# Performance work log

Hardware: AMD Instinct MI355X
Metric: run time of the kernel (lower is better)

## Reference

```python
import jax, jax.numpy as jnp
import numpy as np

IN_CH, PATCH, STRIDE, RES, NCLS = 3, 64, 32, 4096, 1000
SPECTRAL_RADIUS = 0.9


def setup_inputs() -> dict:
    key = jax.random.key(0)
    ks = jax.random.split(key, 8)
    x = jax.random.normal(ks[0], (128, IN_CH, 8224), dtype=jnp.float32)
    # Conv1d weights: [out=PATCH, in=IN_CH, k=PATCH]
    fan_in = IN_CH * PATCH
    bound = 1.0 / np.sqrt(fan_in)
    conv_w = jax.random.uniform(ks[1], (PATCH, IN_CH, PATCH), minval=-bound, maxval=bound, dtype=jnp.float32)
    conv_b = jax.random.uniform(ks[2], (PATCH,), minval=-bound, maxval=bound, dtype=jnp.float32)
    # Reservoir weights (uniform(-0.5, 0.5)), spectral-radius normalized
    rng = np.random.default_rng(0)
    Wres = rng.random((RES, RES), dtype=np.float32) - 0.5
    max_eig = np.max(np.abs(np.linalg.eigvals(Wres)))
    Wres = Wres * (SPECTRAL_RADIUS / max_eig)
    W_reservoir = jnp.asarray(Wres, dtype=jnp.float32)
    W_input = jax.random.uniform(ks[3], (RES, PATCH), minval=-0.5, maxval=0.5, dtype=jnp.float32)
    # cls/dist tokens init to zeros (as in torch)
    cls_token = jnp.zeros((1, PATCH), dtype=jnp.float32)
    dist_token = jnp.zeros((1, PATCH), dtype=jnp.float32)
    hb = 1.0 / np.sqrt(RES)
    w_cls = jax.random.uniform(ks[4], (NCLS, RES), minval=-hb, maxval=hb, dtype=jnp.float32)
    b_cls = jax.random.uniform(ks[5], (NCLS,), minval=-hb, maxval=hb, dtype=jnp.float32)
    w_dist = jax.random.uniform(ks[6], (NCLS, RES), minval=-hb, maxval=hb, dtype=jnp.float32)
    b_dist = jax.random.uniform(ks[7], (NCLS,), minval=-hb, maxval=hb, dtype=jnp.float32)
    return {"x": x, "conv_w": conv_w, "conv_b": conv_b, "W_reservoir": W_reservoir,
            "W_input": W_input, "cls_token": cls_token, "dist_token": dist_token,
            "w_cls": w_cls, "b_cls": b_cls, "w_dist": w_dist, "b_dist": b_dist}


def reference(x, conv_w, conv_b, W_reservoir, W_input, cls_token, dist_token,
              w_cls, b_cls, w_dist, b_dist):
    B = x.shape[0]
    # PatchEmbed: conv1d -> [B, PATCH, L]
    feat = jax.lax.conv_general_dilated(
        x, conv_w, window_strides=(STRIDE,), padding='VALID',
        dimension_numbers=('NCH', 'OIH', 'NCH')) + conv_b[None, :, None]
    WinT = W_input.T  # [PATCH, RES]
    us = jnp.transpose(feat, (2, 0, 1))  # [L, B, PATCH]
    h0 = jnp.zeros((B, RES), dtype=x.dtype)

    def step(h, u):
        h = jnp.tanh(h @ W_reservoir + u @ WinT)
        return h, None

    h, _ = jax.lax.scan(step, h0, us)
    cls_tok = jnp.broadcast_to(cls_token, (B, PATCH))
    dist_tok = jnp.broadcast_to(dist_token, (B, PATCH))
    h_cls = jnp.tanh(h @ W_reservoir + cls_tok @ WinT)
    h_dist = jnp.tanh(h @ W_reservoir + dist_tok @ WinT)
    cls_out = h_cls @ w_cls.T + b_cls
    dist_out = h_dist @ w_dist.T + b_dist
    # eval mode: log_softmax of the averaged logits
    return jax.nn.log_softmax((cls_out + dist_out) * 0.5, axis=1)
```

## Files before the change

kernel.cpp:

```cpp
#include <hip/hip_runtime.h>
#include <hip/hip_bf16.h>

#define LSTEPS 256

typedef short  bf16x8_t  __attribute__((ext_vector_type(8)));
typedef float  f32x4_t   __attribute__((ext_vector_type(4)));
typedef unsigned short us4_t __attribute__((ext_vector_type(4)));
typedef unsigned short us8_t __attribute__((ext_vector_type(8)));

static __device__ __forceinline__ unsigned short f2bf(float f) {
  unsigned int u = __float_as_uint(f);
  unsigned int r = (u + 0x7fffu + ((u >> 16) & 1u)) >> 16;
  return (unsigned short)r;
}
static __device__ __forceinline__ float bf2f(unsigned short s) {
  return __uint_as_float(((unsigned int)s) << 16);
}
static __device__ __forceinline__ float tanh_fast(float x) {
  float e = __expf(2.f * x);
  return 1.f - 2.f / (e + 1.f);
}

#define GLD(dst, off, sbase)                                              \
  asm volatile("global_load_dwordx4 %0, %1, %2 sc0"                       \
               : "=v"(dst)                                                \
               : "v"(off), "s"(sbase)                                     \
               : "memory");

__global__ __launch_bounds__(256) void prep_wc_kernel(
    const float* __restrict__ wcls, const float* __restrict__ wdist,
    unsigned short* __restrict__ Wcat)
{
  const int row = blockIdx.x;
  const float* src = nullptr;
  if (row < 1000) src = wcls + (size_t)row * 4096;
  else if (row >= 1024 && row < 2024) src = wdist + (size_t)(row - 1024) * 4096;
  unsigned short* dst = Wcat + (size_t)row * 4096;
  #pragma unroll 4
  for (int r = 0; r < 16; ++r) {
    const int c = r * 256 + threadIdx.x;
    dst[c] = src ? f2bf(src[c]) : (unsigned short)0;
  }
}

__global__ __launch_bounds__(256) void conv_kernel(
    const float* __restrict__ x, const float* __restrict__ w,
    const float* __restrict__ bias, unsigned short* __restrict__ U)
{
  __shared__ float wl[192][64];
  const int b  = blockIdx.x >> 4;
  const int tg = blockIdx.x & 15;
  const int tid = threadIdx.x;
  for (int i = tid; i < 64 * 192; i += 256)
    wl[i % 192][i / 192] = w[i];
  __syncthreads();
  const int wv = tid >> 6, p = tid & 63;
  const float* xb = x + (size_t)b * (3 * 8224);
  const float bp = bias[p];
  for (int tt = 0; tt < 4; ++tt) {
    const int t = tg * 16 + wv * 4 + tt;
    float acc = bp;
    const float* xw = xb + t * 32;
    #pragma unroll
    for (int c = 0; c < 3; ++c)
      #pragma unroll 8
      for (int k = 0; k < 64; ++k)
        acc += xw[c * 8224 + k] * wl[c * 64 + k][p];
    U[((size_t)t * 8 + (p >> 3)) * 1024 + (size_t)b * 8 + (p & 7)] = f2bf(acc);
  }
}

__global__ __launch_bounds__(256) void prep_tok_kernel(
    const float* __restrict__ cls, const float* __restrict__ dist,
    unsigned short* __restrict__ U)
{
  const int i = blockIdx.x * 256 + threadIdx.x;
  const int s = i >> 13, rem = i & 8191;
  const int kg = rem >> 10, e = rem & 7;
  const float* tok = s ? dist : cls;
  U[(size_t)(256 + s) * 8192 + rem] = f2bf(tok[kg * 8 + e]);
}

__global__ __launch_bounds__(512, 1) void reservoir_persistent(
    const float* __restrict__ wres,
    const unsigned short* __restrict__ U,
    const float* __restrict__ winp,
    unsigned short* __restrict__ A0, unsigned short* __restrict__ A1,
    unsigned short* __restrict__ Hcls, unsigned short* __restrict__ Hdist,
    unsigned int* __restrict__ lcnt, unsigned int* __restrict__ gcnt,
    unsigned int* __restrict__ lgo)
{
  extern __shared__ char smem[];
  unsigned short* Wl = (unsigned short*)smem;

  const int bid  = blockIdx.x;
  const int tid  = threadIdx.x;
  const int w    = tid >> 6;
  const int lane = tid & 63;
  const int q    = lane >> 4;
  const int l15  = lane & 15;
  const int grp  = bid & 7;
  const int nbase = bid * 16;

  {
    const int c4 = (tid & 3) * 4;
    for (int k = tid >> 2; k < 4096; k += 128) {
      float4 v = *(const float4*)(wres + (size_t)k * 4096 + nbase + c4);
      unsigned short* dst = Wl + ((k >> 3) * 16 + c4) * 8 + (k & 7);
      dst[0]  = f2bf(v.x); dst[8]  = f2bf(v.y);
      dst[16] = f2bf(v.z); dst[24] = f2bf(v.w);
    }
    if (tid < 128) {
      const int kg_u = tid >> 4, col = tid & 15;
      const float* src = winp + (size_t)(nbase + col) * 64 + kg_u * 8;
      unsigned short* dst = Wl + ((512 + kg_u) * 16 + col) * 8;
      #pragma unroll
      for (int e = 0; e < 8; ++e) dst[e] = f2bf(src[e]);
    }
  }
  __syncthreads();

  const unsigned int vbase = (unsigned int)(q * 2048 + (w * 16 + l15) * 16);
  unsigned int phase = 0;

#define ISSUE_A(BUF, CO)                                                     \
  { const unsigned int o_ = vbase + (unsigned int)(CO) * 32768u;             \
    GLD(BUF[0], o_, Ar);                                                     \
    GLD(BUF[1], o_ + 8192u, Ar);                                             \
    GLD(BUF[2], o_ + 16384u, Ar);                                            \
    GLD(BUF[3], o_ + 24576u, Ar); }

#define ISSUE_U(BUF)                                                         \
  { GLD(BUF[0], vbase, Ut);                                                  \
    GLD(BUF[1], vbase + 8192u, Ut); }

#define MMW(BUF, CI, VN)                                                     \
  { const unsigned short* wp_ = Wl + (unsigned int)(CI) * 2048 + q * 128 + l15 * 8; \
    bf16x8_t w0_ = *(const bf16x8_t*)(wp_);                                  \
    bf16x8_t w1_ = *(const bf16x8_t*)(wp_ + 512);                            \
    bf16x8_t w2_ = *(const bf16x8_t*)(wp_ + 1024);                           \
    bf16x8_t w3_ = *(const bf16x8_t*)(wp_ + 1536);                           \
    asm volatile("s_waitcnt vmcnt(" #VN ")" ::: "memory");                   \
    __builtin_amdgcn_sched_barrier(0);                                       \
    acc = __builtin_amdgcn_mfma_f32_16x16x32_bf16(BUF[0], w0_, acc, 0, 0, 0);\
    acc = __builtin_amdgcn_mfma_f32_16x16x32_bf16(BUF[1], w1_, acc, 0, 0, 0);\
    acc = __builtin_amdgcn_mfma_f32_16x16x32_bf16(BUF[2], w2_, acc, 0, 0, 0);\
    acc = __builtin_amdgcn_mfma_f32_16x16x32_bf16(BUF[3], w3_, acc, 0, 0, 0); }

  #pragma unroll 1
  for (int t = 0; t < LSTEPS + 2; ++t) {
    const unsigned short* Arp = (t <= LSTEPS) ? ((t & 1) ? A1 : A0) : A0;
    unsigned short* Awp = ((t + 1) & 1) ? A1 : A0;
    const unsigned long long Ar = (unsigned long long)Arp;
    const unsigned long long Ut = (unsigned long long)(U + (size_t)t * 8192);

    f32x4_t acc = (f32x4_t){0.f, 0.f, 0.f, 0.f};
    bf16x8_t b0[4], b1[4], b2[4];

    ISSUE_A(b0, 0); ISSUE_A(b1, 1); ISSUE_A(b2, 2);

    int ci = 0;
    #pragma unroll 1
    for (int ii = 0; ii < 9; ++ii) {
      MMW(b0, ci,     8); ISSUE_A(b0, ci + 3);
      MMW(b1, ci + 1, 8); ISSUE_A(b1, ci + 4);
      MMW(b2, ci + 2, 8); ISSUE_A(b2, ci + 5);
      ci += 3;
    }
    MMW(b0, 27, 8); ISSUE_A(b0, 30);
    MMW(b1, 28, 8); ISSUE_A(b1, 31);
    MMW(b2, 29, 8); ISSUE_U(b2);
    MMW(b0, 30, 6);
    MMW(b1, 31, 2);
    {
      const unsigned short* wp_ = Wl + 65536 + q * 128 + l15 * 8;
      bf16x8_t w0_ = *(const bf16x8_t*)(wp_);
      bf16x8_t w1_ = *(const bf16x8_t*)(wp_ + 512);
      asm volatile("s_waitcnt vmcnt(0)" ::: "memory");
      __builtin_amdgcn_sched_barrier(0);
      acc = __builtin_amdgcn_mfma_f32_16x16x32_bf16(b2[0], w0_, acc, 0, 0, 0);
      acc = __builtin_amdgcn_mfma_f32_16x16x32_bf16(b2[1], w1_, acc, 0, 0, 0);
    }

    {
      const int grow = w * 16 + q * 4;
      if (t < LSTEPS) {
        const int kg_out = bid * 2 + (l15 >> 3);
        unsigned short* dst = Awp + ((size_t)kg_out * 128 + grow) * 8 + (l15 & 7);
        dst[0]  = f2bf(tanh_fast(acc[0]));
        dst[8]  = f2bf(tanh_fast(acc[1]));
        dst[16] = f2bf(tanh_fast(acc[2]));
        dst[24] = f2bf(tanh_fast(acc[3]));
      } else {
        unsigned short* H = (t == LSTEPS) ? Hcls : Hdist;
        unsigned short* dst = H + (size_t)grow * 4096 + nbase + l15;
        dst[0]     = f2bf(tanh_fast(acc[0]));
        dst[4096]  = f2bf(tanh_fast(acc[1]));
        dst[8192]  = f2bf(tanh_fast(acc[2]));
        dst[12288] = f2bf(tanh_fast(acc[3]));
      }
    }

    phase += 1;
    __syncthreads();
    if (tid == 0) {
      unsigned int prev = __hip_atomic_fetch_add(&lcnt[grp * 32], 1u,
                            __ATOMIC_RELAXED, __HIP_MEMORY_SCOPE_AGENT);
      if (prev == phase * 32u - 1u) {
        __hip_atomic_fetch_add(gcnt, 1u, __ATOMIC_RELEASE, __HIP_MEMORY_SCOPE_AGENT);
        while (__hip_atomic_load(gcnt, __ATOMIC_RELAXED, __HIP_MEMORY_SCOPE_SYSTEM)
               < phase * 8u)
          __builtin_amdgcn_s_sleep(1);
        (void)__hip_atomic_load(gcnt, __ATOMIC_ACQUIRE, __HIP_MEMORY_SCOPE_AGENT);
        __hip_atomic_store(&lgo[grp * 32], phase,
                           __ATOMIC_RELAXED, __HIP_MEMORY_SCOPE_AGENT);
      } else {
        while (__hip_atomic_load(&lgo[grp * 32], __ATOMIC_RELAXED,
                                 __HIP_MEMORY_SCOPE_SYSTEM) < phase)
          __builtin_amdgcn_s_sleep(1);
      }
    }
    __syncthreads();
  }
#undef ISSUE_A
#undef ISSUE_U
#undef MMW
}

__global__ __launch_bounds__(256) void gemm_ksplit(
    const unsigned short* __restrict__ A0, const unsigned short* __restrict__ A1,
    int nsplit, int lda,
    const unsigned short* __restrict__ BT, int ldb,
    float* __restrict__ P, int ntiles, int klen, int klen_last)
{
  __shared__ unsigned short sA[128 * 64];
  __shared__ unsigned short sB[128 * 64];

  const int bid = blockIdx.x;
  const int nt = bid % ntiles;
  const int s  = bid / ntiles;
  const unsigned short* __restrict__ A = (nt < nsplit) ? A0 : A1;
  const int kb0 = s * klen;
  const int KL  = (s == 7) ? klen_last : klen;
  const int nbase = nt * 128;

  const int tid = threadIdx.x;
  const int w = tid >> 6;
  const int lane = tid & 63;
  const int wr = w >> 1, wc = w & 1;

  f32x4_t acc[4][4];
  #pragma unroll
  for (int m = 0; m < 4; ++m)
    #pragma unroll
    for (int n = 0; n < 4; ++n)
      acc[m][n] = (f32x4_t){0.f, 0.f, 0.f, 0.f};

  const int srow = lane >> 3;
  const int slotL = (lane & 7) ^ srow;

  for (int kb = 0; kb < KL; kb += 64) {
    const int kcol = kb0 + kb + slotL * 8;
    #pragma unroll
    for (int qq = 0; qq < 4; ++qq) {
      const int row = 32 * w + 8 * qq + srow;
      __builtin_amdgcn_global_load_lds(
          (const __attribute__((address_space(1))) void*)(A + (size_t)row * lda + kcol),
          (__attribute__((address_space(3))) void*)(&sA[(32 * w + 8 * qq) * 64]),
          16, 0, 0);
      __builtin_amdgcn_global_load_lds(
          (const __attribute__((address_space(1))) void*)(BT + (size_t)(nbase + row) * ldb + kcol),
          (__attribute__((address_space(3))) void*)(&sB[(32 * w + 8 * qq) * 64]),
          16, 0, 0);
    }
    __syncthreads();

    #pragma unroll
    for (int ksub = 0; ksub < 2; ++ksub) {
      bf16x8_t af[4], bfr[4];
      #pragma unroll
      for (int m = 0; m < 4; ++m) {
        const int row = 64 * wr + 16 * m + (lane & 15);
        const int kslot = (ksub * 4 + (lane >> 4)) ^ (row & 7);
        af[m] = *(const bf16x8_t*)(&sA[row * 64 + kslot * 8]);
      }
      #pragma unroll
      for (int n = 0; n < 4; ++n) {
        const int row = 64 * wc + 16 * n + (lane & 15);
        const int kslot = (ksub * 4 + (lane >> 4)) ^ (row & 7);
        bfr[n] = *(const bf16x8_t*)(&sB[row * 64 + kslot * 8]);
      }
      #pragma unroll
      for (int m = 0; m < 4; ++m)
        #pragma unroll
        for (int n = 0; n < 4; ++n)
          acc[m][n] = __builtin_amdgcn_mfma_f32_16x16x32_bf16(af[m], bfr[n], acc[m][n], 0, 0, 0);
    }
    __syncthreads();
  }

  float* __restrict__ Pp = P + (size_t)s * (128 * 4096);
  #pragma unroll
  for (int m = 0; m < 4; ++m) {
    const int rbase = 64 * wr + 16 * m + ((lane >> 4) << 2);
    #pragma unroll
    for (int n = 0; n < 4; ++n) {
      const int col = nbase + 64 * wc + 16 * n + (lane & 15);
      #pragma unroll
      for (int r = 0; r < 4; ++r)
        Pp[(size_t)(rbase + r) * 4096 + col] = acc[m][n][r];
    }
  }
}

__global__ __launch_bounds__(256) void reduce_linear_kernel(
    const float* __restrict__ P, float* __restrict__ logits)
{
  const int e = blockIdx.x * 1024 + threadIdx.x * 4;
  const int b = e >> 11;
  const int n = e & 2047;
  const size_t off = (size_t)b * 4096 + n;
  float4 sum = *(const float4*)(&P[off]);
  #pragma unroll
  for (int s = 1; s < 8; ++s) {
    float4 v = *(const float4*)(&P[(size_t)s * 524288 + off]);
    sum.x += v.x; sum.y += v.y; sum.z += v.z; sum.w += v.w;
  }
  *(float4*)(&logits[e]) = sum;
}

__global__ __launch_bounds__(256) void logsoftmax_kernel(
    const float* __restrict__ logits, const float* __restrict__ bcls,
    const float* __restrict__ bdist, float* __restrict__ out)
{
  __shared__ float v[1000];
  __shared__ float red[256];
  const int b = blockIdx.x;
  const int tid = threadIdx.x;
  float lmax = -1e30f;
  for (int n = tid; n < 1000; n += 256) {
    float val = 0.5f * (logits[(size_t)b * 2048 + n] + bcls[n]
                      + logits[(size_t)b * 2048 + 1024 + n] + bdist[n]);
    v[n] = val;
    lmax = fmaxf(lmax, val);
  }
  red[tid] = lmax; __syncthreads();
  for (int st = 128; st > 0; st >>= 1) {
    if (tid < st) red[tid] = fmaxf(red[tid], red[tid + st]);
    __syncthreads();
  }
  const float mx = red[0];
  __syncthreads();
  float lsum = 0.f;
  for (int n = tid; n < 1000; n += 256) lsum += expf(v[n] - mx);
  red[tid] = lsum; __syncthreads();
  for (int st = 128; st > 0; st >>= 1) {
    if (tid < st) red[tid] += red[tid + st];
    __syncthreads();
  }
  const float lse = logf(red[0]) + mx;
  for (int n = tid; n < 1000; n += 256) out[(size_t)b * 1000 + n] = v[n] - lse;
}

extern "C" void kernel_launch(void* const* d_in, const int* in_sizes, int n_in,
                              void* d_out, int out_size, void* d_ws, size_t ws_size,
                              hipStream_t stream)
{
  (void)in_sizes; (void)n_in; (void)out_size; (void)ws_size;
  const float* x      = (const float*)d_in[0];
  const float* convw  = (const float*)d_in[1];
  const float* convb  = (const float*)d_in[2];
  const float* wres   = (const float*)d_in[3];
  const float* winp   = (const float*)d_in[4];
  const float* clstok = (const float*)d_in[5];
  const float* dsttok = (const float*)d_in[6];
  const float* wcls   = (const float*)d_in[7];
  const float* bcls   = (const float*)d_in[8];
  const float* wdist  = (const float*)d_in[9];
  const float* bdist  = (const float*)d_in[10];
  float* out = (float*)d_out;

  char* ws = (char*)d_ws;
  unsigned short* U     = (unsigned short*)(ws + 0);
  unsigned short* A0    = (unsigned short*)(ws + 4227072);
  unsigned short* A1    = (unsigned short*)(ws + 5275648);
  unsigned short* Hcls  = (unsigned short*)(ws + 6324224);
  unsigned short* Hdist = (unsigned short*)(ws + 7372800);
  unsigned short* Wcat  = (unsigned short*)(ws + 8421376);
  float*          P     = (float*)(ws + 25198592);
  float*          logit = (float*)(ws + 41975808);
  unsigned int*   lcnt  = (unsigned int*)(ws + 43024384);
  unsigned int*   lgo   = (unsigned int*)(ws + 43025408);
  unsigned int*   gcnt  = (unsigned int*)(ws + 43026432);

  hipFuncSetAttribute((const void*)reservoir_persistent,
                      hipFuncAttributeMaxDynamicSharedMemorySize, 133120);

  hipMemsetAsync(A0, 0, 2 * 1048576, stream);
  hipMemsetAsync(lcnt, 0, 4096, stream);

  prep_wc_kernel<<<2048, 256, 0, stream>>>(wcls, wdist, Wcat);
  conv_kernel<<<2048, 256, 0, stream>>>(x, convw, convb, U);
  prep_tok_kernel<<<64, 256, 0, stream>>>(clstok, dsttok, U);

  reservoir_persistent<<<256, 512, 133120, stream>>>(
      wres, U, winp, A0, A1, Hcls, Hdist, lcnt, gcnt, lgo);

  gemm_ksplit<<<128, 256, 0, stream>>>(Hcls, Hdist, 8, 4096, Wcat, 4096, P, 16, 512, 512);
  reduce_linear_kernel<<<256, 256, 0, stream>>>(P, logit);
  logsoftmax_kernel<<<128, 256, 0, stream>>>(logit, bcls, bdist, out);
}
```

Baseline: 3.367 ms.

## Keep reservoir weights in registers and split K across waves with LDS reduction

The persistent reservoir kernel is restructured. Each block now owns 32 output columns and half the batch, and each wave keeps its K-slice of the bf16 reservoir weights resident in registers instead of in LDS. Partial sums from the 8 waves are reduced through a padded LDS buffer before tanh and a vectorized store. The hand-written asm global loads with explicit waitcnt pipelining are dropped in favour of plain loads, and the LDS footprint shrinks, so launch bounds now allow two blocks per CU. The risks are heavy register pressure from 32 bf16x8 weight fragments, an extra LDS round-trip and barrier on every step, and the loss of the explicit load/MFMA overlap.

```diff
diff --git a/kernel.cpp b/kernel.cpp
--- a/kernel.cpp
+++ b/kernel.cpp
@@ -6,26 +6,16 @@
 typedef short  bf16x8_t  __attribute__((ext_vector_type(8)));
 typedef float  f32x4_t   __attribute__((ext_vector_type(4)));
 typedef unsigned short us4_t __attribute__((ext_vector_type(4)));
-typedef unsigned short us8_t __attribute__((ext_vector_type(8)));
 
 static __device__ __forceinline__ unsigned short f2bf(float f) {
   unsigned int u = __float_as_uint(f);
   unsigned int r = (u + 0x7fffu + ((u >> 16) & 1u)) >> 16;
   return (unsigned short)r;
 }
-static __device__ __forceinline__ float bf2f(unsigned short s) {
-  return __uint_as_float(((unsigned int)s) << 16);
-}
 static __device__ __forceinline__ float tanh_fast(float x) {
   float e = __expf(2.f * x);
   return 1.f - 2.f / (e + 1.f);
 }
-
-#define GLD(dst, off, sbase)                                              \
-  asm volatile("global_load_dwordx4 %0, %1, %2 sc0"                       \
-               : "=v"(dst)                                                \
-               : "v"(off), "s"(sbase)                                     \
-               : "memory");
 
 __global__ __launch_bounds__(256) void prep_wc_kernel(
     const float* __restrict__ wcls, const float* __restrict__ wdist,
@@ -81,7 +71,7 @@
   U[(size_t)(256 + s) * 8192 + rem] = f2bf(tok[kg * 8 + e]);
 }
 
-__global__ __launch_bounds__(512, 1) void reservoir_persistent(
+__global__ __launch_bounds__(512, 2) void reservoir_persistent(
     const float* __restrict__ wres,
     const unsigned short* __restrict__ U,
     const float* __restrict__ winp,
@@ -91,113 +81,147 @@
     unsigned int* __restrict__ lgo)
 {
   extern __shared__ char smem[];
-  unsigned short* Wl = (unsigned short*)smem;
+  float* Pl = (float*)smem;
+  unsigned short* Wu = (unsigned short*)(smem + 67584);
 
   const int bid  = blockIdx.x;
   const int tid  = threadIdx.x;
   const int w    = tid >> 6;
   const int lane = tid & 63;
   const int q    = lane >> 4;
-  const int l15  = lane & 15;
+  const int r    = lane & 15;
+  const int cg   = bid >> 1;
+  const int bh   = bid & 1;
+  const int nbase = cg * 32;
   const int grp  = bid & 7;
-  const int nbase = bid * 16;
-
-  {
-    const int c4 = (tid & 3) * 4;
-    for (int k = tid >> 2; k < 4096; k += 128) {
-      float4 v = *(const float4*)(wres + (size_t)k * 4096 + nbase + c4);
-      unsigned short* dst = Wl + ((k >> 3) * 16 + c4) * 8 + (k & 7);
-      dst[0]  = f2bf(v.x); dst[8]  = f2bf(v.y);
-      dst[16] = f2bf(v.z); dst[24] = f2bf(v.w);
-    }
-    if (tid < 128) {
-      const int kg_u = tid >> 4, col = tid & 15;
-      const float* src = winp + (size_t)(nbase + col) * 64 + kg_u * 8;
-      unsigned short* dst = Wl + ((512 + kg_u) * 16 + col) * 8;
-      #pragma unroll
-      for (int e = 0; e < 8; ++e) dst[e] = f2bf(src[e]);
-    }
-  }
-  __syncthreads();
-
-  const unsigned int vbase = (unsigned int)(q * 2048 + (w * 16 + l15) * 16);
+
+  bf16x8_t wf[16][2];
+  #pragma unroll
+  for (int kk = 0; kk < 16; ++kk)
+    #pragma unroll
+    for (int ct = 0; ct < 2; ++ct) {
+      const float* src = wres + (size_t)(w * 512 + kk * 32 + q * 8) * 4096
+                              + nbase + ct * 16 + r;
+      bf16x8_t f;
+      #pragma unroll
+      for (int e = 0; e < 8; ++e) f[e] = (short)f2bf(src[(size_t)e * 4096]);
+      wf[kk][ct] = f;
+    }
+  if (w < 2) {
+    #pragma unroll
+    for (int ct = 0; ct < 2; ++ct) {
+      const float* src = winp + (size_t)(nbase + ct * 16 + r) * 64 + w * 32 + q * 8;
+      bf16x8_t f;
+      #pragma unroll
+      for (int e = 0; e < 8; ++e) f[e] = (short)f2bf(src[e]);
+      *(bf16x8_t*)(Wu + ((size_t)(ct * 2 + w) * 64 + lane) * 8) = f;
+    }
+  }
+
+  const int au = (w * 64 + q) * 128 + bh * 64 + r;
+  const int uu = (w * 4 + q) * 128 + bh * 64 + r;
+
+  const int erow = tid >> 3;
+  const int cb   = (tid & 7) * 4;
+  const size_t awoff = ((size_t)(cg * 4 + (cb >> 3)) * 128 + bh * 64 + erow) * 8 + (cb & 7);
+  const size_t hoff  = (size_t)(bh * 64 + erow) * 4096 + nbase + cb;
+
   unsigned int phase = 0;
 
-#define ISSUE_A(BUF, CO)                                                     \
-  { const unsigned int o_ = vbase + (unsigned int)(CO) * 32768u;             \
-    GLD(BUF[0], o_, Ar);                                                     \
-    GLD(BUF[1], o_ + 8192u, Ar);                                             \
-    GLD(BUF[2], o_ + 16384u, Ar);                                            \
-    GLD(BUF[3], o_ + 24576u, Ar); }
-
-#define ISSUE_U(BUF)                                                         \
-  { GLD(BUF[0], vbase, Ut);                                                  \
-    GLD(BUF[1], vbase + 8192u, Ut); }
-
-#define MMW(BUF, CI, VN)                                                     \
-  { const unsigned short* wp_ = Wl + (unsigned int)(CI) * 2048 + q * 128 + l15 * 8; \
-    bf16x8_t w0_ = *(const bf16x8_t*)(wp_);                                  \
-    bf16x8_t w1_ = *(const bf16x8_t*)(wp_ + 512);                            \
-    bf16x8_t w2_ = *(const bf16x8_t*)(wp_ + 1024);                           \
-    bf16x8_t w3_ = *(const bf16x8_t*)(wp_ + 1536);                           \
-    asm volatile("s_waitcnt vmcnt(" #VN ")" ::: "memory");                   \
-    __builtin_amdgcn_sched_barrier(0);                                       \
-    acc = __builtin_amdgcn_mfma_f32_16x16x32_bf16(BUF[0], w0_, acc, 0, 0, 0);\
-    acc = __builtin_amdgcn_mfma_f32_16x16x32_bf16(BUF[1], w1_, acc, 0, 0, 0);\
-    acc = __builtin_amdgcn_mfma_f32_16x16x32_bf16(BUF[2], w2_, acc, 0, 0, 0);\
-    acc = __builtin_amdgcn_mfma_f32_16x16x32_bf16(BUF[3], w3_, acc, 0, 0, 0); }
+#define LD(BUF, KK)                                                          \
+  { BUF[0] = Ab[au + (KK) * 512];      BUF[1] = Ab[au + (KK) * 512 + 16];    \
+    BUF[2] = Ab[au + (KK) * 512 + 32]; BUF[3] = Ab[au + (KK) * 512 + 48]; }
+
+#define MMc(BUF, KK)                                                         \
+  { acc[0][0] = __builtin_amdgcn_mfma_f32_16x16x32_bf16(BUF[0], wf[KK][0], acc[0][0], 0, 0, 0); \
+    acc[0][1] = __builtin_amdgcn_mfma_f32_16x16x32_bf16(BUF[0], wf[KK][1], acc[0][1], 0, 0, 0); \
+    acc[1][0] = __builtin_amdgcn_mfma_f32_16x16x32_bf16(BUF[1], wf[KK][0], acc[1][0], 0, 0, 0); \
+    acc[1][1] = __builtin_amdgcn_mfma_f32_16x16x32_bf16(BUF[1], wf[KK][1], acc[1][1], 0, 0, 0); \
+    acc[2][0] = __builtin_amdgcn_mfma_f32_16x16x32_bf16(BUF[2], wf[KK][0], acc[2][0], 0, 0, 0); \
+    acc[2][1] = __builtin_amdgcn_mfma_f32_16x16x32_bf16(BUF[2], wf[KK][1], acc[2][1], 0, 0, 0); \
+    acc[3][0] = __builtin_amdgcn_mfma_f32_16x16x32_bf16(BUF[3], wf[KK][0], acc[3][0], 0, 0, 0); \
+    acc[3][1] = __builtin_amdgcn_mfma_f32_16x16x32_bf16(BUF[3], wf[KK][1], acc[3][1], 0, 0, 0); }
+
+#define MMU(BUF, WU0, WU1)                                                   \
+  { acc[0][0] = __builtin_amdgcn_mfma_f32_16x16x32_bf16(BUF[0], WU0, acc[0][0], 0, 0, 0); \
+    acc[0][1] = __builtin_amdgcn_mfma_f32_16x16x32_bf16(BUF[0], WU1, acc[0][1], 0, 0, 0); \
+    acc[1][0] = __builtin_amdgcn_mfma_f32_16x16x32_bf16(BUF[1], WU0, acc[1][0], 0, 0, 0); \
+    acc[1][1] = __builtin_amdgcn_mfma_f32_16x16x32_bf16(BUF[1], WU1, acc[1][1], 0, 0, 0); \
+    acc[2][0] = __builtin_amdgcn_mfma_f32_16x16x32_bf16(BUF[2], WU0, acc[2][0], 0, 0, 0); \
+    acc[2][1] = __builtin_amdgcn_mfma_f32_16x16x32_bf16(BUF[2], WU1, acc[2][1], 0, 0, 0); \
+    acc[3][0] = __builtin_amdgcn_mfma_f32_16x16x32_bf16(BUF[3], WU0, acc[3][0], 0, 0, 0); \
+    acc[3][1] = __builtin_amdgcn_mfma_f32_16x16x32_bf16(BUF[3], WU1, acc[3][1], 0, 0, 0); }
 
   #pragma unroll 1
   for (int t = 0; t < LSTEPS + 2; ++t) {
     const unsigned short* Arp = (t <= LSTEPS) ? ((t & 1) ? A1 : A0) : A0;
     unsigned short* Awp = ((t + 1) & 1) ? A1 : A0;
-    const unsigned long long Ar = (unsigned long long)Arp;
-    const unsigned long long Ut = (unsigned long long)(U + (size_t)t * 8192);
-
-    f32x4_t acc = (f32x4_t){0.f, 0.f, 0.f, 0.f};
-    bf16x8_t b0[4], b1[4], b2[4];
-
-    ISSUE_A(b0, 0); ISSUE_A(b1, 1); ISSUE_A(b2, 2);
-
-    int ci = 0;
-    #pragma unroll 1
-    for (int ii = 0; ii < 9; ++ii) {
-      MMW(b0, ci,     8); ISSUE_A(b0, ci + 3);
-      MMW(b1, ci + 1, 8); ISSUE_A(b1, ci + 4);
-      MMW(b2, ci + 2, 8); ISSUE_A(b2, ci + 5);
-      ci += 3;
-    }
-    MMW(b0, 27, 8); ISSUE_A(b0, 30);
-    MMW(b1, 28, 8); ISSUE_A(b1, 31);
-    MMW(b2, 29, 8); ISSUE_U(b2);
-    MMW(b0, 30, 6);
-    MMW(b1, 31, 2);
+    const bf16x8_t* __restrict__ Ab = (const bf16x8_t*)Arp;
+    const bf16x8_t* __restrict__ Ub = (const bf16x8_t*)(U + (size_t)t * 8192);
+
+    f32x4_t acc[4][2];
+    #pragma unroll
+    for (int m = 0; m < 4; ++m) {
+      acc[m][0] = (f32x4_t){0.f, 0.f, 0.f, 0.f};
+      acc[m][1] = (f32x4_t){0.f, 0.f, 0.f, 0.f};
+    }
+
+    bf16x8_t b0[4], b1[4];
+    LD(b0, 0); LD(b1, 1);
+
+    MMc(b0, 0);  LD(b0, 2);
+    MMc(b1, 1);  LD(b1, 3);
+    MMc(b0, 2);  LD(b0, 4);
+    MMc(b1, 3);  LD(b1, 5);
+    MMc(b0, 4);  LD(b0, 6);
+    MMc(b1, 5);  LD(b1, 7);
+    MMc(b0, 6);  LD(b0, 8);
+    MMc(b1, 7);  LD(b1, 9);
+    MMc(b0, 8);  LD(b0, 10);
+    MMc(b1, 9);  LD(b1, 11);
+    MMc(b0, 10); LD(b0, 12);
+    MMc(b1, 11); LD(b1, 13);
+    MMc(b0, 12); LD(b0, 14);
+    MMc(b1, 13); LD(b1, 15);
+    MMc(b0, 14);
+    if (w < 2) {
+      bf16x8_t bu[4];
+      bu[0] = Ub[uu];      bu[1] = Ub[uu + 16];
+      bu[2] = Ub[uu + 32]; bu[3] = Ub[uu + 48];
+      MMc(b1, 15);
+      bf16x8_t wu0 = *(const bf16x8_t*)(Wu + ((size_t)(0 * 2 + w) * 64 + lane) * 8);
+      bf16x8_t wu1 = *(const bf16x8_t*)(Wu + ((size_t)(1 * 2 + w) * 64 + lane) * 8);
+      MMU(bu, wu0, wu1);
+    } else {
+      MMc(b1, 15);
+    }
+
+    #pragma unroll
+    for (int rt = 0; rt < 4; ++rt)
+      #pragma unroll
+      for (int ct = 0; ct < 2; ++ct)
+        #pragma unroll
+        for (int i = 0; i < 4; ++i)
+          Pl[(w * 64 + rt * 16 + q * 4 + i) * 33 + ct * 16 + r] = acc[rt][ct][i];
+    __syncthreads();
+
     {
-      const unsigned short* wp_ = Wl + 65536 + q * 128 + l15 * 8;
-      bf16x8_t w0_ = *(const bf16x8_t*)(wp_);
-      bf16x8_t w1_ = *(const bf16x8_t*)(wp_ + 512);
-      asm volatile("s_waitcnt vmcnt(0)" ::: "memory");
-      __builtin_amdgcn_sched_barrier(0);
-      acc = __builtin_amdgcn_mfma_f32_16x16x32_bf16(b2[0], w0_, acc, 0, 0, 0);
-      acc = __builtin_amdgcn_mfma_f32_16x16x32_bf16(b2[1], w1_, acc, 0, 0, 0);
-    }
-
-    {
-      const int grow = w * 16 + q * 4;
+      float s0 = 0.f, s1 = 0.f, s2 = 0.f, s3 = 0.f;
+      #pragma unroll
+      for (int wv = 0; wv < 8; ++wv) {
+        const float* p = Pl + (wv * 64 + erow) * 33 + cb;
+        s0 += p[0]; s1 += p[1]; s2 += p[2]; s3 += p[3];
+      }
+      us4_t o;
+      o[0] = f2bf(tanh_fast(s0));
+      o[1] = f2bf(tanh_fast(s1));
+      o[2] = f2bf(tanh_fast(s2));
+      o[3] = f2bf(tanh_fast(s3));
       if (t < LSTEPS) {
-        const int kg_out = bid * 2 + (l15 >> 3);
-        unsigned short* dst = Awp + ((size_t)kg_out * 128 + grow) * 8 + (l15 & 7);
-        dst[0]  = f2bf(tanh_fast(acc[0]));
-        dst[8]  = f2bf(tanh_fast(acc[1]));
-        dst[16] = f2bf(tanh_fast(acc[2]));
-        dst[24] = f2bf(tanh_fast(acc[3]));
+        *(us4_t*)(Awp + awoff) = o;
       } else {
         unsigned short* H = (t == LSTEPS) ? Hcls : Hdist;
-        unsigned short* dst = H + (size_t)grow * 4096 + nbase + l15;
-        dst[0]     = f2bf(tanh_fast(acc[0]));
-        dst[4096]  = f2bf(tanh_fast(acc[1]));
-        dst[8192]  = f2bf(tanh_fast(acc[2]));
-        dst[12288] = f2bf(tanh_fast(acc[3]));
+        *(us4_t*)(H + hoff) = o;
       }
     }
 
@@ -222,9 +246,9 @@
     }
     __syncthreads();
   }
-#undef ISSUE_A
-#undef ISSUE_U
-#undef MMW
+#undef LD
+#undef MMc
+#undef MMU
 }
 
 __global__ __launch_bounds__(256) void gemm_ksplit(
@@ -394,7 +418,7 @@
   unsigned int*   gcnt  = (unsigned int*)(ws + 43026432);
 
   hipFuncSetAttribute((const void*)reservoir_persistent,
-                      hipFuncAttributeMaxDynamicSharedMemorySize, 133120);
+                      hipFuncAttributeMaxDynamicSharedMemorySize, 71680);
 
   hipMemsetAsync(A0, 0, 2 * 1048576, stream);
   hipMemsetAsync(lcnt, 0, 4096, stream);
@@ -403,7 +427,7 @@
   conv_kernel<<<2048, 256, 0, stream>>>(x, convw, convb, U);
   prep_tok_kernel<<<64, 256, 0, stream>>>(clstok, dsttok, U);
 
-  reservoir_persistent<<<256, 512, 133120, stream>>>(
+  reservoir_persistent<<<256, 512, 71680, stream>>>(
       wres, U, winp, A0, A1, Hcls, Hdist, lcnt, gcnt, lgo);
 
   gemm_ksplit<<<128, 256, 0, stream>>>(Hcls, Hdist, 8, 4096, Wcat, 4096, P, 16, 512, 512);
```

After: 3.142 ms. 6.7% less time.
